# Performance work log

Measured on AMD Instinct MI355X. Metric: run time of the kernel, lower is better.

The kernel has to match this reference:

```python
import jax, jax.numpy as jnp
import numpy as np

NC = 80          # class_num
THRESH = 0.5     # objectness threshold (forward arg `thresh`)
IOU_T = 0.3      # NMS IoU threshold (utils.nms(boxes_c, 0.3))
K = 512          # fixed candidate budget per image (jit-safe replacement for nonzero)


def _decode(out, t, anchors):
    """_filter + _parse for one scale. out: (B, 3*(5+NC), H, W) -> boxes (B, H*W*3, 6), conf (B, H*W*3).
    Box columns: x1, y1, x2, y2, conf, cls."""
    B, C, H, W = out.shape
    o = out.transpose(0, 2, 3, 1).reshape(B, H, W, 3, 5 + NC)
    txy = jax.nn.sigmoid(o[..., 0:2])          # sigmoid on tx, ty
    conf = jax.nn.sigmoid(o[..., 4])           # sigmoid on objectness
    gy = jnp.arange(H, dtype=out.dtype)[:, None, None]   # grid row index (idxs[:,1])
    gx = jnp.arange(W, dtype=out.dtype)[None, :, None]   # grid col index (idxs[:,2])
    cy = (gy + txy[..., 1]) * t
    cx = (gx + txy[..., 0]) * t
    w = anchors[:, 0] * jnp.exp(o[..., 2])     # anchors broadcast over anchor axis
    h = anchors[:, 1] * jnp.exp(o[..., 3])
    cls = jnp.argmax(o[..., 5:], axis=-1).astype(out.dtype)
    boxes = jnp.stack([cx - w / 2, cy - h / 2, cx + w / 2, cy + h / 2, conf, cls], axis=-1)
    return boxes.reshape(B, -1, 6), conf.reshape(B, -1)


def _iou(b):
    """Pairwise IoU. b: (B, K, 4) -> (B, K, K)."""
    x1, y1, x2, y2 = b[..., 0], b[..., 1], b[..., 2], b[..., 3]
    area = (x2 - x1) * (y2 - y1)
    ix1 = jnp.maximum(x1[:, :, None], x1[:, None, :])
    iy1 = jnp.maximum(y1[:, :, None], y1[:, None, :])
    ix2 = jnp.minimum(x2[:, :, None], x2[:, None, :])
    iy2 = jnp.minimum(y2[:, :, None], y2[:, None, :])
    inter = jnp.maximum(ix2 - ix1, 0.0) * jnp.maximum(iy2 - iy1, 0.0)
    return inter / (area[:, :, None] + area[:, None, :] - inter + 1e-9)


def setup_inputs() -> dict:
    key = jax.random.key(0)
    k1, k2, k3 = jax.random.split(key, 3)
    B, C = 32, 3 * (5 + NC)
    return {
        "out13": jax.random.normal(k1, (B, C, 13, 13), jnp.float32),
        "out26": jax.random.normal(k2, (B, C, 26, 26), jnp.float32),
        "out52": jax.random.normal(k3, (B, C, 52, 52), jnp.float32),
        "anchors13": jnp.array([[116.0, 90.0], [156.0, 198.0], [373.0, 326.0]], jnp.float32),
        "anchors26": jnp.array([[30.0, 61.0], [62.0, 45.0], [59.0, 119.0]], jnp.float32),
        "anchors52": jnp.array([[10.0, 13.0], [16.0, 30.0], [33.0, 23.0]], jnp.float32),
    }


def reference(out13, out26, out52, anchors13, anchors26, anchors52):
    b13, c13 = _decode(out13, 32.0, anchors13)
    b26, c26 = _decode(out26, 16.0, anchors26)
    b52, c52 = _decode(out52, 8.0, anchors52)
    boxes = jnp.concatenate([b13, b26, b52], axis=1)   # (B, N, 6), N = 3549*3
    conf = jnp.concatenate([c13, c26, c52], axis=1)    # (B, N)
    B = boxes.shape[0]

    # threshold filter (conf > thresh) realized as masked top-K (jit-safe nonzero)
    scores = jnp.where(conf > THRESH, conf, -1.0)
    vals, idx = jax.lax.top_k(scores, K)               # sorted descending, as utils.nms expects
    bk = jnp.take_along_axis(boxes, idx[..., None], axis=1)   # (B, K, 6)
    valid = vals > THRESH                              # (B, K)

    # per-class greedy NMS
    iou = _iou(bk[..., :4])                            # (B, K, K)
    same_cls = bk[..., 5][:, :, None] == bk[..., 5][:, None, :]
    suppress = same_cls & (iou > IOU_T)

    def step(keep, i):
        sup_i = jnp.any(keep & suppress[:, i, :], axis=-1)
        keep = keep.at[:, i].set(valid[:, i] & ~sup_i)
        return keep, None

    keep, _ = jax.lax.scan(step, jnp.zeros((B, K), dtype=bool), jnp.arange(K))
    # (B, K, 7): x1, y1, x2, y2, conf, cls, keep_flag
    return jnp.concatenate([bk, keep[..., None].astype(bk.dtype)], axis=-1)
```

## Files before the change

kernel.cpp:

```cpp
#include <hip/hip_runtime.h>
#include <stdint.h>

#define NC13 507
#define NC26 2028
#define NC52 8112
#define NCAND 10647
#define KSEL 512
#define POOLCAP 768
#define POOLTGT 640
#define SUPW 17
#define CMW 17
#define DECB 6

__device__ __forceinline__ unsigned long long cand_key(
    int i, int b,
    const float* __restrict__ in13,
    const float* __restrict__ in26,
    const float* __restrict__ in52)
{
    const float* in; int HW, base;
    if (i < NC13)              { in = in13; HW = 169;  base = 0; }
    else if (i < NC13 + NC26)  { in = in26; HW = 676;  base = NC13; }
    else                       { in = in52; HW = 2704; base = NC13 + NC26; }
    const int within = i - base;
    const int a  = within / HW;
    const int hw = within - a * HW;
    const float xo = in[((size_t)b * 255 + (size_t)a * 85 + 4) * HW + hw];
    const int n = base + hw * 3 + a;
    const unsigned long long low = (unsigned long long)(0x3FFFu - (unsigned)n);
    return (xo > 0.0f)
        ? ((1ull << 63) | ((unsigned long long)__float_as_uint(xo) << 32) | low)
        : low;
}

struct SelShared {
    unsigned int hist[4096];
    unsigned long long pool[POOLCAP];
    unsigned int cnt;
    unsigned long long prefix;
    unsigned long long tmin;
    int krem, shift, brk, V;
};

__device__ __forceinline__ void decode_write(
    float* __restrict__ o, int w, int h, float ts,
    float tx, float ty, float tw, float th, float xo,
    float aw, float ah, int cls)
{
    const float sx   = 1.0f / (1.0f + expf(-tx));
    const float sy   = 1.0f / (1.0f + expf(-ty));
    const float conf = 1.0f / (1.0f + expf(-xo));
    const float cx = ((float)w + sx) * ts;
    const float cy = ((float)h + sy) * ts;
    const float bw = aw * expf(tw);
    const float bh = ah * expf(th);
    o[0] = cx - bw * 0.5f; o[1] = cy - bh * 0.5f;
    o[2] = cx + bw * 0.5f; o[3] = cy + bh * 0.5f;
    o[4] = conf; o[5] = (float)cls;
}

__device__ __forceinline__ void decode4(
    const float* __restrict__ in, const float* __restrict__ anch,
    int b, int a, int hw, int HW, int Hdim, float ts, int base,
    float* __restrict__ boxesAll)
{
    const int HW4 = HW >> 2;
    const float4* p4 = reinterpret_cast<const float4*>(
        in + ((size_t)b * 255 + (size_t)a * 85) * HW + hw);

    const float4 txv = p4[0];
    const float4 tyv = p4[(size_t)HW4];
    const float4 twv = p4[(size_t)2 * HW4];
    const float4 thv = p4[(size_t)3 * HW4];
    const float4 xov = p4[(size_t)4 * HW4];

    float4 best = make_float4(-INFINITY, -INFINITY, -INFINITY, -INFINITY);
    int bx = 0, by = 0, bz = 0, bw4 = 0;

    float4 vb[4];
    #pragma unroll
    for (int j = 0; j < 4; ++j) vb[j] = p4[(size_t)(5 + j) * HW4];
    for (int cb = 0; cb < 20; ++cb) {
        float4 vn[4];
        if (cb < 19) {
            #pragma unroll
            for (int j = 0; j < 4; ++j) vn[j] = p4[(size_t)(9 + cb * 4 + j) * HW4];
        }
        #pragma unroll
        for (int j = 0; j < 4; ++j) {
            const int c = cb * 4 + j;
            if (vb[j].x > best.x) { best.x = vb[j].x; bx = c; }
            if (vb[j].y > best.y) { best.y = vb[j].y; by = c; }
            if (vb[j].z > best.z) { best.z = vb[j].z; bz = c; }
            if (vb[j].w > best.w) { best.w = vb[j].w; bw4 = c; }
        }
        #pragma unroll
        for (int j = 0; j < 4; ++j) vb[j] = vn[j];
    }

    const float aw = anch[2 * a], ah = anch[2 * a + 1];
    const int i0 = base + a * HW + hw;
    float* o = boxesAll + ((size_t)b * NCAND + i0) * 6;
    {
        const int h = hw / Hdim, w = hw - h * Hdim;
        decode_write(o, w, h, ts, txv.x, tyv.x, twv.x, thv.x, xov.x, aw, ah, bx);
    }
    {
        const int h = (hw + 1) / Hdim, w = (hw + 1) - h * Hdim;
        decode_write(o + 6, w, h, ts, txv.y, tyv.y, twv.y, thv.y, xov.y, aw, ah, by);
    }
    {
        const int h = (hw + 2) / Hdim, w = (hw + 2) - h * Hdim;
        decode_write(o + 12, w, h, ts, txv.z, tyv.z, twv.z, thv.z, xov.z, aw, ah, bz);
    }
    {
        const int h = (hw + 3) / Hdim, w = (hw + 3) - h * Hdim;
        decode_write(o + 18, w, h, ts, txv.w, tyv.w, twv.w, thv.w, xov.w, aw, ah, bw4);
    }
}

__global__ __launch_bounds__(512, 2) void main_kernel(
    const float* __restrict__ in13,
    const float* __restrict__ in26,
    const float* __restrict__ in52,
    const float* __restrict__ a13,
    const float* __restrict__ a26,
    const float* __restrict__ a52,
    int B,
    int* __restrict__ selidx,
    int* __restrict__ selv,
    float* __restrict__ boxesAll)
{
    __shared__ __align__(16) char smem_raw[sizeof(SelShared)];
    const int bid = blockIdx.x;
    const int tid = threadIdx.x;

    if (bid < B) {
        SelShared& S = *reinterpret_cast<SelShared*>(smem_raw);
        const int b = bid;
        if (tid == 0) { S.cnt = 0; S.prefix = 0; S.krem = KSEL; S.shift = 52; S.brk = 0; S.V = 0; }
        __syncthreads();

        for (int i = tid; i < NCAND; i += 512) {
            const unsigned long long k = cand_key(i, b, in13, in26, in52);
            const unsigned long long bal = __ballot((k >> 63) != 0ull);
            if ((tid & 63) == 0) atomicAdd(&S.V, (int)__popcll(bal));
        }
        __syncthreads();
        const bool include = (S.V < KSEL);

        while (true) {
            const int shift = S.shift;
            const unsigned long long prefix = S.prefix;
            const int krem = S.krem;
            __syncthreads();
            for (int i = tid; i < 4096; i += 512) S.hist[i] = 0;
            __syncthreads();
            for (int i = tid; i < NCAND; i += 512) {
                const unsigned long long k = cand_key(i, b, in13, in26, in52);
                const bool part = include || ((k >> 63) != 0ull);
                const bool ok = part &&
                    ((shift == 52) || ((k >> (shift + 12)) == prefix));
                if (ok) atomicAdd(&S.hist[(unsigned)((k >> shift) & 0xFFFull)], 1u);
            }
            __syncthreads();
            if (tid < 64) {
                unsigned int s = 0;
                for (int q = 0; q < 64; ++q) s += S.hist[tid * 64 + q];
                unsigned int suf = s;
                for (int off = 1; off < 64; off <<= 1) {
                    const unsigned int v = __shfl_down(suf, off);
                    if (tid + off < 64) suf += v;
                }
                const unsigned long long ball = __ballot(suf >= (unsigned)krem);
                const int lstar = 63 - __clzll(ball);
                const unsigned int base = (lstar < 63) ? __shfl(suf, lstar + 1) : 0u;
                const unsigned int wv = S.hist[lstar * 64 + (63 - tid)];
                unsigned int pv = wv;
                for (int off = 1; off < 64; off <<= 1) {
                    const unsigned int v = __shfl_up(pv, off);
                    if (tid >= (unsigned)off) pv += v;
                }
                const unsigned long long b2 = __ballot(base + pv >= (unsigned)krem);
                const int mstar = __ffsll(b2) - 1;
                const unsigned int pvm = __shfl(pv, mstar);
                const unsigned int wvm = __shfl(wv, mstar);
                if (tid == 0) {
                    const int dstar = lstar * 64 + (63 - mstar);
                    const unsigned long long np = (prefix << 12) | (unsigned long long)dstar;
                    const int Albl = (int)(base + pvm - wvm);
                    const int Cpool = (KSEL - krem) + Albl + (int)wvm;
                    S.prefix = np;
                    S.krem = krem - Albl;
                    if (Cpool <= POOLTGT || shift == 4) {
                        S.brk = 1;
                        S.tmin = np << shift;
                    } else {
                        S.shift = shift - 12;
                    }
                }
            }
            __syncthreads();
            if (S.brk) break;
        }
        const unsigned long long tmin = S.tmin;

        for (int i = tid; i < NCAND; i += 512) {
            const unsigned long long k = cand_key(i, b, in13, in26, in52);
            if (k >= tmin) {
                const unsigned int p = atomicAdd(&S.cnt, 1u);
                if (p < POOLCAP) S.pool[p] = k;
            }
        }
        __syncthreads();
        const int C = ((int)S.cnt < POOLCAP) ? (int)S.cnt : POOLCAP;

        for (int p = tid; p < C; p += 512) {
            const unsigned long long k = S.pool[p];
            int r = 0;
            for (int j = 0; j < C; ++j) r += (S.pool[j] > k) ? 1 : 0;
            if (r < KSEL) {
                const int idx = 0x3FFF - (int)(k & 0x3FFFull);
                selidx[(size_t)b * KSEL + r] = idx;
                selv[(size_t)b * KSEL + r]   = (int)(k >> 63);
            }
        }
        return;
    }

    const int d = bid - B;
    const int b = d / DECB;
    const int role = d - b * DECB;

    if (role < 4) {
        const int idx4 = role * 512 + tid;
        if (idx4 < 3 * 676) {
            const int a = idx4 / 676, g = idx4 - a * 676;
            decode4(in52, a52, b, a, g * 4, 2704, 52, 8.f, NC13 + NC26, boxesAll);
        }
    } else if (role == 4) {
        if (tid < 3 * 169) {
            const int a = tid / 169, g = tid - a * 169;
            decode4(in26, a26, b, a, g * 4, 676, 26, 16.f, NC13, boxesAll);
        }
    } else {
        if (tid < NC13) {
            const int HW = 169;
            const int a = tid / HW, hw = tid - a * HW;
            const int h = hw / 13, w = hw - h * 13;
            const float* p = in13 + ((size_t)b * 255 + (size_t)a * 85) * HW + hw;
            const float tx = p[0];
            const float ty = p[(size_t)HW];
            const float tw = p[(size_t)2 * HW];
            const float th = p[(size_t)3 * HW];
            const float xo = p[(size_t)4 * HW];
            float best = -INFINITY; int bi = 0;
            float vb[4];
            #pragma unroll
            for (int j = 0; j < 4; ++j) vb[j] = p[(size_t)(5 + j) * HW];
            for (int cb = 0; cb < 20; ++cb) {
                float vn[4];
                if (cb < 19) {
                    #pragma unroll
                    for (int j = 0; j < 4; ++j) vn[j] = p[(size_t)(9 + cb * 4 + j) * HW];
                }
                #pragma unroll
                for (int j = 0; j < 4; ++j) {
                    const int c = cb * 4 + j;
                    if (vb[j] > best) { best = vb[j]; bi = c; }
                }
                #pragma unroll
                for (int j = 0; j < 4; ++j) vb[j] = vn[j];
            }
            const int i = a * HW + hw;
            decode_write(boxesAll + ((size_t)b * NCAND + i) * 6, w, h, 32.f,
                         tx, ty, tw, th, xo, a13[2 * a], a13[2 * a + 1], bi);
        }
    }
}

__global__ __launch_bounds__(512) void nms_kernel(
    const float* __restrict__ boxesAll,
    const int* __restrict__ selidx,
    const int* __restrict__ selv,
    float* __restrict__ out)
{
    __shared__ float X1[KSEL], Y1[KSEL], X2[KSEL], Y2[KSEL], AR[KSEL];
    __shared__ int CLS[KSEL];
    __shared__ unsigned int CM[80 * CMW];
    __shared__ unsigned int SUP[KSEL * SUPW];
    __shared__ unsigned int KEEP[16];
    __shared__ int shV;

    const int b = blockIdx.x;
    const int tid = threadIdx.x;

    const int n = selidx[(size_t)b * KSEL + tid];
    int base, HW;
    if (n < NC13)             { base = 0;           HW = 169; }
    else if (n < NC13 + NC26) { base = NC13;        HW = 676; }
    else                      { base = NC13 + NC26; HW = 2704; }
    const int within = n - base;
    const int hw = within / 3, a = within - 3 * hw;
    const int i = base + a * HW + hw;
    const float* src = boxesAll + ((size_t)b * NCAND + i) * 6;
    const float x1 = src[0], y1 = src[1], x2 = src[2], y2 = src[3];
    const float conf = src[4], clsf = src[5];
    const float ar = (x2 - x1) * (y2 - y1);
    const int ci = (int)clsf;
    X1[tid] = x1; Y1[tid] = y1; X2[tid] = x2; Y2[tid] = y2;
    AR[tid] = ar; CLS[tid] = ci;
    const int v = selv[(size_t)b * KSEL + tid];
    if (tid == 0) shV = 0;
    for (int q = tid; q < 80 * CMW; q += KSEL) CM[q] = 0;
    __syncthreads();

    atomicOr(&CM[ci * CMW + (tid >> 5)], 1u << (tid & 31));
    const unsigned long long bal = __ballot(v != 0);
    if ((tid & 63) == 0) atomicAdd(&shV, __popcll(bal));
    __syncthreads();

    for (int wj = 0; wj < 16; ++wj) {
        unsigned int m = CM[ci * CMW + wj];
        unsigned int bits = 0;
        while (m) {
            const int bit = __ffs(m) - 1;
            m &= m - 1;
            const int j = wj * 32 + bit;
            const float iw = fminf(x2, X2[j]) - fmaxf(x1, X1[j]);
            const float ih = fminf(y2, Y2[j]) - fmaxf(y1, Y1[j]);
            if (iw > 0.0f && ih > 0.0f) {
                const float inter = iw * ih;
                if (inter > 0.3f * (ar + AR[j] - inter + 1e-9f))
                    bits |= (1u << bit);
            }
        }
        SUP[tid * SUPW + wj] = bits;
    }
    __syncthreads();

    if (tid < 64) {
        const int V = shV;
        unsigned int keepw = 0;
        unsigned int buf[16];
        #pragma unroll
        for (int r = 0; r < 16; ++r)
            buf[r] = (tid < 16) ? SUP[r * SUPW + tid] : 0u;
        for (int g = 0; g < 32; ++g) {
            unsigned int nbuf[16] = {0};
            if (g < 31) {
                #pragma unroll
                for (int r = 0; r < 16; ++r)
                    nbuf[r] = (tid < 16) ? SUP[((g + 1) * 16 + r) * SUPW + tid] : 0u;
            }
            #pragma unroll
            for (int r = 0; r < 16; ++r) {
                const int ii = g * 16 + r;
                const bool anysup = __any((keepw & buf[r]) != 0u);
                const bool ki = (ii < V) && !anysup;
                if (ki && tid == (ii >> 5)) keepw |= (1u << (ii & 31));
            }
            #pragma unroll
            for (int r = 0; r < 16; ++r) buf[r] = nbuf[r];
        }
        if (tid < 16) KEEP[tid] = keepw;
    }
    __syncthreads();

    const float kf = ((KEEP[tid >> 5] >> (tid & 31)) & 1u) ? 1.0f : 0.0f;
    float* dst = out + ((size_t)b * KSEL + tid) * 7;
    dst[0] = x1; dst[1] = y1; dst[2] = x2;
    dst[3] = y2; dst[4] = conf; dst[5] = clsf;
    dst[6] = kf;
}

extern "C" void kernel_launch(void* const* d_in, const int* in_sizes, int n_in,
                              void* d_out, int out_size, void* d_ws, size_t ws_size,
                              hipStream_t stream)
{
    (void)n_in; (void)out_size; (void)ws_size;
    const float* in13 = (const float*)d_in[0];
    const float* in26 = (const float*)d_in[1];
    const float* in52 = (const float*)d_in[2];
    const float* a13  = (const float*)d_in[3];
    const float* a26  = (const float*)d_in[4];
    const float* a52  = (const float*)d_in[5];
    float* out = (float*)d_out;
    const int B = in_sizes[0] / (255 * 169);

    char* w = (char*)d_ws;
    int* selidx = (int*)w;  w += ((size_t)B * KSEL * sizeof(int) + 255) & ~(size_t)255;
    int* selv   = (int*)w;  w += ((size_t)B * KSEL * sizeof(int) + 255) & ~(size_t)255;
    float* boxesAll = (float*)w;
    w += ((size_t)B * NCAND * 6 * sizeof(float) + 255) & ~(size_t)255;

    main_kernel<<<dim3(B * (1 + DECB)), 512, 0, stream>>>(
        in13, in26, in52, a13, a26, a52, B, selidx, selv, boxesAll);
    nms_kernel<<<dim3(B), 512, 0, stream>>>(boxesAll, selidx, selv, out);
}
```

Before: 84.22 us.

## Emit compact sort keys during decode and fuse top-K selection into NMS kernel

Decode blocks now also write a packed 64-bit sort key per candidate to workspace. The radix top-K selection moves out of the decode kernel into the NMS kernel, which reads the contiguous keys instead of re-gathering strided objectness values from the inputs on every pass. This takes selection off the decode kernel's critical path and drops the separate valid-count pass by folding it into the first histogram. In exchange, selection now runs serially before NMS in the second kernel, and the extra key array adds global write and read traffic.

```diff
diff --git a/kernel.cpp b/kernel.cpp
--- a/kernel.cpp
+++ b/kernel.cpp
@@ -12,35 +12,12 @@
 #define CMW 17
 #define DECB 6
 
-__device__ __forceinline__ unsigned long long cand_key(
-    int i, int b,
-    const float* __restrict__ in13,
-    const float* __restrict__ in26,
-    const float* __restrict__ in52)
-{
-    const float* in; int HW, base;
-    if (i < NC13)              { in = in13; HW = 169;  base = 0; }
-    else if (i < NC13 + NC26)  { in = in26; HW = 676;  base = NC13; }
-    else                       { in = in52; HW = 2704; base = NC13 + NC26; }
-    const int within = i - base;
-    const int a  = within / HW;
-    const int hw = within - a * HW;
-    const float xo = in[((size_t)b * 255 + (size_t)a * 85 + 4) * HW + hw];
-    const int n = base + hw * 3 + a;
+__device__ __forceinline__ unsigned long long make_key(float xo, int n) {
     const unsigned long long low = (unsigned long long)(0x3FFFu - (unsigned)n);
     return (xo > 0.0f)
         ? ((1ull << 63) | ((unsigned long long)__float_as_uint(xo) << 32) | low)
         : low;
 }
-
-struct SelShared {
-    unsigned int hist[4096];
-    unsigned long long pool[POOLCAP];
-    unsigned int cnt;
-    unsigned long long prefix;
-    unsigned long long tmin;
-    int krem, shift, brk, V;
-};
 
 __device__ __forceinline__ void decode_write(
     float* __restrict__ o, int w, int h, float ts,
@@ -62,7 +39,7 @@
 __device__ __forceinline__ void decode4(
     const float* __restrict__ in, const float* __restrict__ anch,
     int b, int a, int hw, int HW, int Hdim, float ts, int base,
-    float* __restrict__ boxesAll)
+    float* __restrict__ boxesAll, unsigned long long* __restrict__ keys)
 {
     const int HW4 = HW >> 2;
     const float4* p4 = reinterpret_cast<const float4*>(
@@ -98,6 +75,12 @@
         for (int j = 0; j < 4; ++j) vb[j] = vn[j];
     }
 
+    unsigned long long* kb = keys + (size_t)b * NCAND;
+    kb[base + (hw + 0) * 3 + a] = make_key(xov.x, base + (hw + 0) * 3 + a);
+    kb[base + (hw + 1) * 3 + a] = make_key(xov.y, base + (hw + 1) * 3 + a);
+    kb[base + (hw + 2) * 3 + a] = make_key(xov.z, base + (hw + 2) * 3 + a);
+    kb[base + (hw + 3) * 3 + a] = make_key(xov.w, base + (hw + 3) * 3 + a);
+
     const float aw = anch[2 * a], ah = anch[2 * a + 1];
     const int i0 = base + a * HW + hw;
     float* o = boxesAll + ((size_t)b * NCAND + i0) * 6;
@@ -119,129 +102,30 @@
     }
 }
 
-__global__ __launch_bounds__(512, 2) void main_kernel(
+__global__ __launch_bounds__(512, 2) void decode_kernel(
     const float* __restrict__ in13,
     const float* __restrict__ in26,
     const float* __restrict__ in52,
     const float* __restrict__ a13,
     const float* __restrict__ a26,
     const float* __restrict__ a52,
-    int B,
-    int* __restrict__ selidx,
-    int* __restrict__ selv,
-    float* __restrict__ boxesAll)
+    float* __restrict__ boxesAll,
+    unsigned long long* __restrict__ keys)
 {
-    __shared__ __align__(16) char smem_raw[sizeof(SelShared)];
-    const int bid = blockIdx.x;
+    const int role = blockIdx.x;
+    const int b = blockIdx.y;
     const int tid = threadIdx.x;
-
-    if (bid < B) {
-        SelShared& S = *reinterpret_cast<SelShared*>(smem_raw);
-        const int b = bid;
-        if (tid == 0) { S.cnt = 0; S.prefix = 0; S.krem = KSEL; S.shift = 52; S.brk = 0; S.V = 0; }
-        __syncthreads();
-
-        for (int i = tid; i < NCAND; i += 512) {
-            const unsigned long long k = cand_key(i, b, in13, in26, in52);
-            const unsigned long long bal = __ballot((k >> 63) != 0ull);
-            if ((tid & 63) == 0) atomicAdd(&S.V, (int)__popcll(bal));
-        }
-        __syncthreads();
-        const bool include = (S.V < KSEL);
-
-        while (true) {
-            const int shift = S.shift;
-            const unsigned long long prefix = S.prefix;
-            const int krem = S.krem;
-            __syncthreads();
-            for (int i = tid; i < 4096; i += 512) S.hist[i] = 0;
-            __syncthreads();
-            for (int i = tid; i < NCAND; i += 512) {
-                const unsigned long long k = cand_key(i, b, in13, in26, in52);
-                const bool part = include || ((k >> 63) != 0ull);
-                const bool ok = part &&
-                    ((shift == 52) || ((k >> (shift + 12)) == prefix));
-                if (ok) atomicAdd(&S.hist[(unsigned)((k >> shift) & 0xFFFull)], 1u);
-            }
-            __syncthreads();
-            if (tid < 64) {
-                unsigned int s = 0;
-                for (int q = 0; q < 64; ++q) s += S.hist[tid * 64 + q];
-                unsigned int suf = s;
-                for (int off = 1; off < 64; off <<= 1) {
-                    const unsigned int v = __shfl_down(suf, off);
-                    if (tid + off < 64) suf += v;
-                }
-                const unsigned long long ball = __ballot(suf >= (unsigned)krem);
-                const int lstar = 63 - __clzll(ball);
-                const unsigned int base = (lstar < 63) ? __shfl(suf, lstar + 1) : 0u;
-                const unsigned int wv = S.hist[lstar * 64 + (63 - tid)];
-                unsigned int pv = wv;
-                for (int off = 1; off < 64; off <<= 1) {
-                    const unsigned int v = __shfl_up(pv, off);
-                    if (tid >= (unsigned)off) pv += v;
-                }
-                const unsigned long long b2 = __ballot(base + pv >= (unsigned)krem);
-                const int mstar = __ffsll(b2) - 1;
-                const unsigned int pvm = __shfl(pv, mstar);
-                const unsigned int wvm = __shfl(wv, mstar);
-                if (tid == 0) {
-                    const int dstar = lstar * 64 + (63 - mstar);
-                    const unsigned long long np = (prefix << 12) | (unsigned long long)dstar;
-                    const int Albl = (int)(base + pvm - wvm);
-                    const int Cpool = (KSEL - krem) + Albl + (int)wvm;
-                    S.prefix = np;
-                    S.krem = krem - Albl;
-                    if (Cpool <= POOLTGT || shift == 4) {
-                        S.brk = 1;
-                        S.tmin = np << shift;
-                    } else {
-                        S.shift = shift - 12;
-                    }
-                }
-            }
-            __syncthreads();
-            if (S.brk) break;
-        }
-        const unsigned long long tmin = S.tmin;
-
-        for (int i = tid; i < NCAND; i += 512) {
-            const unsigned long long k = cand_key(i, b, in13, in26, in52);
-            if (k >= tmin) {
-                const unsigned int p = atomicAdd(&S.cnt, 1u);
-                if (p < POOLCAP) S.pool[p] = k;
-            }
-        }
-        __syncthreads();
-        const int C = ((int)S.cnt < POOLCAP) ? (int)S.cnt : POOLCAP;
-
-        for (int p = tid; p < C; p += 512) {
-            const unsigned long long k = S.pool[p];
-            int r = 0;
-            for (int j = 0; j < C; ++j) r += (S.pool[j] > k) ? 1 : 0;
-            if (r < KSEL) {
-                const int idx = 0x3FFF - (int)(k & 0x3FFFull);
-                selidx[(size_t)b * KSEL + r] = idx;
-                selv[(size_t)b * KSEL + r]   = (int)(k >> 63);
-            }
-        }
-        return;
-    }
-
-    const int d = bid - B;
-    const int b = d / DECB;
-    const int role = d - b * DECB;
 
     if (role < 4) {
         const int idx4 = role * 512 + tid;
         if (idx4 < 3 * 676) {
             const int a = idx4 / 676, g = idx4 - a * 676;
-            decode4(in52, a52, b, a, g * 4, 2704, 52, 8.f, NC13 + NC26, boxesAll);
+            decode4(in52, a52, b, a, g * 4, 2704, 52, 8.f, NC13 + NC26, boxesAll, keys);
         }
     } else if (role == 4) {
         if (tid < 3 * 169) {
             const int a = tid / 169, g = tid - a * 169;
-            decode4(in26, a26, b, a, g * 4, 676, 26, 16.f, NC13, boxesAll);
+            decode4(in26, a26, b, a, g * 4, 676, 26, 16.f, NC13, boxesAll, keys);
         }
     } else {
         if (tid < NC13) {
@@ -272,6 +156,8 @@
                 #pragma unroll
                 for (int j = 0; j < 4; ++j) vb[j] = vn[j];
             }
+            const int n = hw * 3 + a;
+            keys[(size_t)b * NCAND + n] = make_key(xo, n);
             const int i = a * HW + hw;
             decode_write(boxesAll + ((size_t)b * NCAND + i) * 6, w, h, 32.f,
                          tx, ty, tw, th, xo, a13[2 * a], a13[2 * a + 1], bi);
@@ -279,23 +165,143 @@
     }
 }
 
-__global__ __launch_bounds__(512) void nms_kernel(
+struct SelS {
+    unsigned int hist[4096];
+    unsigned long long pool[POOLCAP];
+    unsigned int cnt;
+    unsigned long long prefix;
+    unsigned long long tmin;
+    int krem, shift, brk, include;
+};
+struct NmsS {
+    float X1[KSEL], Y1[KSEL], X2[KSEL], Y2[KSEL], AR[KSEL];
+    int CLS[KSEL];
+    unsigned int CM[80 * CMW];
+    unsigned int SUP[KSEL * SUPW];
+    unsigned int KEEP[16];
+};
+
+__global__ __launch_bounds__(512) void selnms_kernel(
+    const unsigned long long* __restrict__ keys,
     const float* __restrict__ boxesAll,
-    const int* __restrict__ selidx,
-    const int* __restrict__ selv,
     float* __restrict__ out)
 {
-    __shared__ float X1[KSEL], Y1[KSEL], X2[KSEL], Y2[KSEL], AR[KSEL];
-    __shared__ int CLS[KSEL];
-    __shared__ unsigned int CM[80 * CMW];
-    __shared__ unsigned int SUP[KSEL * SUPW];
-    __shared__ unsigned int KEEP[16];
-    __shared__ int shV;
+    constexpr size_t USZ = sizeof(SelS) > sizeof(NmsS) ? sizeof(SelS) : sizeof(NmsS);
+    __shared__ __align__(16) char smem[USZ];
+    __shared__ int selidxL[KSEL];
+    __shared__ int shVtot;
 
     const int b = blockIdx.x;
     const int tid = threadIdx.x;
-
-    const int n = selidx[(size_t)b * KSEL + tid];
+    const unsigned long long* kb = keys + (size_t)b * NCAND;
+
+    {
+        SelS& S = *reinterpret_cast<SelS*>(smem);
+        if (tid == 0) { S.cnt = 0; S.prefix = 0; S.krem = KSEL; S.shift = 52; S.brk = 0; S.include = 0; }
+        __syncthreads();
+
+        bool first = true;
+        while (true) {
+            const int shift = S.shift;
+            const unsigned long long prefix = S.prefix;
+            const int krem = S.krem;
+            const int include = S.include;
+            __syncthreads();
+            for (int i = tid; i < 4096; i += 512) S.hist[i] = 0;
+            __syncthreads();
+            for (int i = tid; i < NCAND; i += 512) {
+                const unsigned long long k = kb[i];
+                const bool part = include || ((k >> 63) != 0ull);
+                const bool ok = part &&
+                    ((shift == 52) || ((k >> (shift + 12)) == prefix));
+                if (ok) atomicAdd(&S.hist[(unsigned)((k >> shift) & 0xFFFull)], 1u);
+            }
+            __syncthreads();
+
+            if (first) {
+                if (tid < 64) {
+                    unsigned int s = 0;
+                    for (int q = 0; q < 64; ++q) s += S.hist[tid * 64 + q];
+                    unsigned int suf = s;
+                    for (int off = 1; off < 64; off <<= 1) {
+                        const unsigned int v = __shfl_down(suf, off);
+                        if (tid + off < 64) suf += v;
+                    }
+                    if (tid == 0) shVtot = (int)suf;
+                }
+                __syncthreads();
+                if (tid == 0 && shVtot < KSEL) {
+                    S.hist[0] += (unsigned)(NCAND - shVtot);
+                    S.include = 1;
+                }
+                __syncthreads();
+                first = false;
+            }
+
+            if (tid < 64) {
+                unsigned int s = 0;
+                for (int q = 0; q < 64; ++q) s += S.hist[tid * 64 + q];
+                unsigned int suf = s;
+                for (int off = 1; off < 64; off <<= 1) {
+                    const unsigned int v = __shfl_down(suf, off);
+                    if (tid + off < 64) suf += v;
+                }
+                const unsigned long long ball = __ballot(suf >= (unsigned)krem);
+                const int lstar = 63 - __clzll(ball);
+                const unsigned int base = (lstar < 63) ? __shfl(suf, lstar + 1) : 0u;
+                const unsigned int wv = S.hist[lstar * 64 + (63 - tid)];
+                unsigned int pv = wv;
+                for (int off = 1; off < 64; off <<= 1) {
+                    const unsigned int v = __shfl_up(pv, off);
+                    if (tid >= (unsigned)off) pv += v;
+                }
+                const unsigned long long b2 = __ballot(base + pv >= (unsigned)krem);
+                const int mstar = __ffsll(b2) - 1;
+                const unsigned int pvm = __shfl(pv, mstar);
+                const unsigned int wvm = __shfl(wv, mstar);
+                if (tid == 0) {
+                    const int dstar = lstar * 64 + (63 - mstar);
+                    const unsigned long long np = (prefix << 12) | (unsigned long long)dstar;
+                    const int Albl = (int)(base + pvm - wvm);
+                    const int Cpool = (KSEL - krem) + Albl + (int)wvm;
+                    S.prefix = np;
+                    S.krem = krem - Albl;
+                    if (Cpool <= POOLTGT || shift == 4) {
+                        S.brk = 1;
+                        S.tmin = np << shift;
+                    } else {
+                        S.shift = shift - 12;
+                    }
+                }
+            }
+            __syncthreads();
+            if (S.brk) break;
+        }
+        const unsigned long long tmin = S.tmin;
+
+        for (int i = tid; i < NCAND; i += 512) {
+            const unsigned long long k = kb[i];
+            if (k >= tmin) {
+                const unsigned int p = atomicAdd(&S.cnt, 1u);
+                if (p < POOLCAP) S.pool[p] = k;
+            }
+        }
+        __syncthreads();
+        const int C = ((int)S.cnt < POOLCAP) ? (int)S.cnt : POOLCAP;
+
+        for (int p = tid; p < C; p += 512) {
+            const unsigned long long k = S.pool[p];
+            int r = 0;
+            for (int j = 0; j < C; ++j) r += (S.pool[j] > k) ? 1 : 0;
+            if (r < KSEL) selidxL[r] = 0x3FFF - (int)(k & 0x3FFFull);
+        }
+        __syncthreads();
+    }
+
+    NmsS& M = *reinterpret_cast<NmsS*>(smem);
+    const int V = (shVtot < KSEL) ? shVtot : KSEL;
+
+    const int n = selidxL[tid];
     int base, HW;
     if (n < NC13)             { base = 0;           HW = 169; }
     else if (n < NC13 + NC26) { base = NC13;        HW = 676; }
@@ -308,50 +314,45 @@
     const float conf = src[4], clsf = src[5];
     const float ar = (x2 - x1) * (y2 - y1);
     const int ci = (int)clsf;
-    X1[tid] = x1; Y1[tid] = y1; X2[tid] = x2; Y2[tid] = y2;
-    AR[tid] = ar; CLS[tid] = ci;
-    const int v = selv[(size_t)b * KSEL + tid];
-    if (tid == 0) shV = 0;
-    for (int q = tid; q < 80 * CMW; q += KSEL) CM[q] = 0;
+    M.X1[tid] = x1; M.Y1[tid] = y1; M.X2[tid] = x2; M.Y2[tid] = y2;
+    M.AR[tid] = ar; M.CLS[tid] = ci;
+    for (int q = tid; q < 80 * CMW; q += KSEL) M.CM[q] = 0;
     __syncthreads();
 
-    atomicOr(&CM[ci * CMW + (tid >> 5)], 1u << (tid & 31));
-    const unsigned long long bal = __ballot(v != 0);
-    if ((tid & 63) == 0) atomicAdd(&shV, __popcll(bal));
+    atomicOr(&M.CM[ci * CMW + (tid >> 5)], 1u << (tid & 31));
     __syncthreads();
 
     for (int wj = 0; wj < 16; ++wj) {
-        unsigned int m = CM[ci * CMW + wj];
+        unsigned int m = M.CM[ci * CMW + wj];
         unsigned int bits = 0;
         while (m) {
             const int bit = __ffs(m) - 1;
             m &= m - 1;
             const int j = wj * 32 + bit;
-            const float iw = fminf(x2, X2[j]) - fmaxf(x1, X1[j]);
-            const float ih = fminf(y2, Y2[j]) - fmaxf(y1, Y1[j]);
+            const float iw = fminf(x2, M.X2[j]) - fmaxf(x1, M.X1[j]);
+            const float ih = fminf(y2, M.Y2[j]) - fmaxf(y1, M.Y1[j]);
             if (iw > 0.0f && ih > 0.0f) {
                 const float inter = iw * ih;
-                if (inter > 0.3f * (ar + AR[j] - inter + 1e-9f))
+                if (inter > 0.3f * (ar + M.AR[j] - inter + 1e-9f))
                     bits |= (1u << bit);
             }
         }
-        SUP[tid * SUPW + wj] = bits;
+        M.SUP[tid * SUPW + wj] = bits;
     }
     __syncthreads();
 
     if (tid < 64) {
-        const int V = shV;
         unsigned int keepw = 0;
         unsigned int buf[16];
         #pragma unroll
         for (int r = 0; r < 16; ++r)
-            buf[r] = (tid < 16) ? SUP[r * SUPW + tid] : 0u;
+            buf[r] = (tid < 16) ? M.SUP[r * SUPW + tid] : 0u;
         for (int g = 0; g < 32; ++g) {
             unsigned int nbuf[16] = {0};
             if (g < 31) {
                 #pragma unroll
                 for (int r = 0; r < 16; ++r)
-                    nbuf[r] = (tid < 16) ? SUP[((g + 1) * 16 + r) * SUPW + tid] : 0u;
+                    nbuf[r] = (tid < 16) ? M.SUP[((g + 1) * 16 + r) * SUPW + tid] : 0u;
             }
             #pragma unroll
             for (int r = 0; r < 16; ++r) {
@@ -363,11 +364,11 @@
             #pragma unroll
             for (int r = 0; r < 16; ++r) buf[r] = nbuf[r];
         }
-        if (tid < 16) KEEP[tid] = keepw;
+        if (tid < 16) M.KEEP[tid] = keepw;
     }
     __syncthreads();
 
-    const float kf = ((KEEP[tid >> 5] >> (tid & 31)) & 1u) ? 1.0f : 0.0f;
+    const float kf = ((M.KEEP[tid >> 5] >> (tid & 31)) & 1u) ? 1.0f : 0.0f;
     float* dst = out + ((size_t)b * KSEL + tid) * 7;
     dst[0] = x1; dst[1] = y1; dst[2] = x2;
     dst[3] = y2; dst[4] = conf; dst[5] = clsf;
@@ -389,12 +390,12 @@
     const int B = in_sizes[0] / (255 * 169);
 
     char* w = (char*)d_ws;
-    int* selidx = (int*)w;  w += ((size_t)B * KSEL * sizeof(int) + 255) & ~(size_t)255;
-    int* selv   = (int*)w;  w += ((size_t)B * KSEL * sizeof(int) + 255) & ~(size_t)255;
+    unsigned long long* keys = (unsigned long long*)w;
+    w += ((size_t)B * NCAND * sizeof(unsigned long long) + 255) & ~(size_t)255;
     float* boxesAll = (float*)w;
     w += ((size_t)B * NCAND * 6 * sizeof(float) + 255) & ~(size_t)255;
 
-    main_kernel<<<dim3(B * (1 + DECB)), 512, 0, stream>>>(
-        in13, in26, in52, a13, a26, a52, B, selidx, selv, boxesAll);
-    nms_kernel<<<dim3(B), 512, 0, stream>>>(boxesAll, selidx, selv, out);
-}
+    decode_kernel<<<dim3(DECB, B), 512, 0, stream>>>(
+        in13, in26, in52, a13, a26, a52, boxesAll, keys);
+    selnms_kernel<<<dim3(B), 512, 0, stream>>>(keys, boxesAll, out);
+}
```

After: 90.37 us. 7.3% more time.
